# Kernel tuning notes

Hardware: AMD Instinct MI355X
Metric: run time of the kernel (lower is better)

The kernel has to match this reference:

```python
import jax, jax.numpy as jnp
from jax import lax
import numpy as np

B, N, NPOINT, NSAMPLE = 4, 8192, 1024, 32
RADIUS = 0.2
EPS = 1e-5
C_IN = 16
MLP_DIMS = [(3 + C_IN, 64), (64, 64), (64, 128)]


def setup_inputs() -> dict:
    key = jax.random.key(0)
    ks = jax.random.split(key, 16)
    inp = {
        "xyz": jax.random.uniform(ks[0], (B, N, 3), dtype=jnp.float32),
        "points": jax.random.normal(ks[1], (B, N, C_IN), dtype=jnp.float32),
    }
    for i, (cin, cout) in enumerate(MLP_DIMS, 1):
        inp[f"w{i}"] = jax.random.normal(ks[1 + i], (cout, cin), dtype=jnp.float32) / np.sqrt(cin)
        inp[f"b{i}"] = jnp.zeros((cout,), jnp.float32)
        inp[f"g{i}"] = jnp.ones((cout,), jnp.float32)
        inp[f"be{i}"] = jnp.zeros((cout,), jnp.float32)
    return inp


def fps(xyz, npoint):
    # Farthest point sampling; sequential by nature -> lax.scan over npoint steps.
    # Deterministic start at index 0 (torch version uses a random start).
    b, n, _ = xyz.shape
    def step(carry, _):
        dist, far = carry
        centroid = jnp.take_along_axis(xyz, far[:, None, None], axis=1)  # [B,1,3]
        d = jnp.sum((xyz - centroid) ** 2, -1)                            # [B,N]
        dist = jnp.minimum(dist, d)
        return (dist, jnp.argmax(dist, -1).astype(jnp.int32)), far
    init = (jnp.full((b, n), 1e10, xyz.dtype), jnp.zeros((b,), jnp.int32))
    _, idxs = lax.scan(step, init, None, length=npoint)
    return jnp.transpose(idxs)  # [B, npoint]


def gather2(pts, idx):  # pts [B,N,C], idx [B,S] -> [B,S,C]
    return jnp.take_along_axis(pts, idx[..., None], axis=1)


def gather3(pts, idx):  # pts [B,N,C], idx [B,S,K] -> [B,S,K,C]
    b, s, k = idx.shape
    out = jnp.take_along_axis(pts, idx.reshape(b, s * k)[..., None], axis=1)
    return out.reshape(b, s, k, pts.shape[-1])


def ball_query(radius, nsample, xyz, new_xyz):
    n = xyz.shape[1]
    # [B,S,N] pairwise squared distances (the memory-bound hot spot)
    sqr = jnp.sum((new_xyz[:, :, None, :] - xyz[:, None, :, :]) ** 2, -1)
    gidx = jnp.where(sqr > radius * radius, n, jnp.arange(n, dtype=jnp.int32))
    gidx = jnp.sort(gidx, axis=-1)[:, :, :nsample]
    first = gidx[:, :, :1]
    return jnp.where(gidx == n, first, gidx)


def mlp_layer(x, w, b, g, be):
    # 1x1 Conv2d + BatchNorm2d (train mode: batch stats over B,S,K) + ReLU
    y = jnp.einsum('bskc,oc->bsko', x, w) + b
    mu = jnp.mean(y, axis=(0, 1, 2))
    var = jnp.var(y, axis=(0, 1, 2))
    y = (y - mu) * (g * lax.rsqrt(var + EPS)) + be
    return jax.nn.relu(y)


def reference(xyz, points, w1, b1, g1, be1, w2, b2, g2, be2, w3, b3, g3, be3):
    fps_idx = fps(xyz, NPOINT)                       # [B,S]
    new_xyz = gather2(xyz, fps_idx)                  # [B,S,3]
    idx = ball_query(RADIUS, NSAMPLE, xyz, new_xyz)  # [B,S,K]
    grouped_xyz_norm = gather3(xyz, idx) - new_xyz[:, :, None, :]  # [B,S,K,3]
    grouped_points = gather3(points, idx)            # [B,S,K,C]
    feat = jnp.concatenate([grouped_xyz_norm, grouped_points], -1)  # [B,S,K,3+C]
    feat = mlp_layer(feat, w1, b1, g1, be1)
    feat = mlp_layer(feat, w2, b2, g2, be2)
    feat = mlp_layer(feat, w3, b3, g3, be3)
    new_points = jnp.max(feat, axis=2)               # max-pool over neighbors -> [B,S,128]
    return new_xyz, new_points
```

## Files before the change

kernel.cpp:

```cpp
#include <hip/hip_runtime.h>

#define NB 4
#define NP 8192
#define NS 1024
#define NK 32
#define CNT_ALL 131072.0f

typedef float v2f __attribute__((ext_vector_type(2)));

template <int CTRL>
__device__ __forceinline__ unsigned dpp_max_u32(unsigned m)
{
    unsigned o = (unsigned)__builtin_amdgcn_update_dpp((int)m, (int)m, CTRL, 0xF, 0xF, false);
    return (o > m) ? o : m;
}

template <int CTRL>
__device__ __forceinline__ unsigned long long dpp_max_u64(unsigned long long k)
{
    unsigned lo = (unsigned)k, hi = (unsigned)(k >> 32);
    unsigned olo = (unsigned)__builtin_amdgcn_update_dpp((int)lo, (int)lo, CTRL, 0xF, 0xF, false);
    unsigned ohi = (unsigned)__builtin_amdgcn_update_dpp((int)hi, (int)hi, CTRL, 0xF, 0xF, false);
    unsigned long long o = ((unsigned long long)ohi << 32) | (unsigned long long)olo;
    return (o > k) ? o : k;
}

__global__ __launch_bounds__(512, 2) void fps_kernel(const float* __restrict__ xyz,
                                                     float* __restrict__ newxyz,
                                                     float* __restrict__ st)
{
#pragma clang fp contract(off)
    if (blockIdx.x >= NB) {
        for (int i = threadIdx.x; i < 4096; i += 512) st[i] = 0.f;
        return;
    }
    const int b = blockIdx.x;
    const int tid = threadIdx.x;
    const int lane = tid & 63;
    const int w = tid >> 6;
    const float* xb = xyz + (size_t)b * NP * 3;

    __shared__ float s_px[NP], s_py[NP], s_pz[NP];
    __shared__ unsigned long long s_kv[2][8];

#pragma unroll
    for (int k = 0; k < 16; ++k) {
        const int i = k * 512 + tid;
        s_px[i] = xb[3 * i + 0];
        s_py[i] = xb[3 * i + 1];
        s_pz[i] = xb[3 * i + 2];
    }
    __syncthreads();

    v2f px[8], py[8], pz[8], dist[8];
    const int base = tid << 4;
#pragma unroll
    for (int m = 0; m < 8; ++m) {
        const int p0 = base + 2 * m;
        px[m] = v2f{s_px[p0], s_px[p0 + 1]};
        py[m] = v2f{s_py[p0], s_py[p0 + 1]};
        pz[m] = v2f{s_pz[p0], s_pz[p0 + 1]};
        dist[m] = v2f{1e10f, 1e10f};
    }
    float cx = s_px[0], cy = s_py[0], cz = s_pz[0];
    float* ob = newxyz + (size_t)b * NS * 3;

    for (int it = 0; it < NS; ++it) {
        if (tid == 0) { ob[it * 3 + 0] = cx; ob[it * 3 + 1] = cy; ob[it * 3 + 2] = cz; }
        const v2f cxx = v2f{cx, cx}, cyy = v2f{cy, cy}, czz = v2f{cz, cz};
        float bd0 = -1.0f, bd1 = -1.0f;
        int bj0 = 0, bj1 = 0;
#pragma unroll
        for (int m = 0; m < 8; ++m) {
            v2f dx = px[m] - cxx, dy = py[m] - cyy, dz = pz[m] - czz;
            v2f d = (dx * dx + dy * dy) + dz * dz;
            float d0 = fminf(dist[m].x, d.x);
            float d1 = fminf(dist[m].y, d.y);
            dist[m].x = d0;
            dist[m].y = d1;
            bool t0 = d0 > bd0;
            bd0 = t0 ? d0 : bd0;
            bj0 = t0 ? 2 * m : bj0;
            bool t1 = d1 > bd1;
            bd1 = t1 ? d1 : bd1;
            bj1 = t1 ? 2 * m + 1 : bj1;
        }
        const bool tm = (bd1 > bd0) || ((bd1 == bd0) && (bj1 < bj0));
        const float bd = tm ? bd1 : bd0;
        const int ibest = base + (tm ? bj1 : bj0);
        const unsigned ub = __float_as_uint(bd);
        unsigned m0 = dpp_max_u32<0xB1>(ub);
        m0 = dpp_max_u32<0x4E>(m0);
        m0 = dpp_max_u32<0x141>(m0);
        m0 = dpp_max_u32<0x140>(m0);
        m0 = dpp_max_u32<0x142>(m0);
        m0 = dpp_max_u32<0x143>(m0);
        const unsigned maxbits = (unsigned)__builtin_amdgcn_readlane((int)m0, 63);
        const unsigned long long bm = __ballot(ub == maxbits);
        const int srclane = __ffsll(bm) - 1;
        const int wbi = __builtin_amdgcn_readlane(ibest, srclane);
        if (lane == 0)
            s_kv[it & 1][w] = ((unsigned long long)maxbits << 32) | (unsigned)(NP - 1 - wbi);
        __syncthreads();
        unsigned long long kv = s_kv[it & 1][lane & 7];
        kv = dpp_max_u64<0xB1>(kv);
        kv = dpp_max_u64<0x4E>(kv);
        kv = dpp_max_u64<0x141>(kv);
        const int fi = NP - 1 - (int)(unsigned)(kv & 0xFFFFFFFFull);
        cx = s_px[fi]; cy = s_py[fi]; cz = s_pz[fi];
    }
}

__device__ __forceinline__ void bn_coef(const float* __restrict__ sums,
                                        const float* __restrict__ sqs,
                                        const float* __restrict__ g,
                                        const float* __restrict__ be,
                                        int C, int c, float& sc, float& sh)
{
    float s = 0.f, q = 0.f;
#pragma unroll
    for (int k = 0; k < 8; ++k) { s += sums[k * C + c]; q += sqs[k * C + c]; }
    const float mean = s / CNT_ALL;
    const float var = q / CNT_ALL - mean * mean;
    sc = g[c] / sqrtf(var + 1e-5f);
    sh = be[c] - mean * sc;
}

__global__ __launch_bounds__(256) void phaseA_kernel(
    const float* __restrict__ xyz, const float* __restrict__ pts,
    const float* __restrict__ newxyz,
    const float* __restrict__ w1, const float* __restrict__ b1,
    float* __restrict__ y1, float* __restrict__ st)
{
    __shared__ int   s_ball[8][NK];
    __shared__ float s_feat[256][20];
    __shared__ float s_ps[256], s_pq[256];
    float* sums1 = st;
    float* sqs1 = st + 512;

    const int tid = threadIdx.x;
    const int bk = blockIdx.x;
    const int lane = tid & 63;
    const int wv_id = tid >> 6;

    const int b = (8 * bk) >> 10;
    const float* xb = xyz + (size_t)b * NP * 3;
    const float rr = (float)(0.2 * 0.2);
    for (int r = 0; r < 2; ++r) {
        const int lg = 2 * wv_id + r;
        const int sg = 8 * bk + lg;
        const float cx = newxyz[sg * 3 + 0];
        const float cy = newxyz[sg * 3 + 1];
        const float cz = newxyz[sg * 3 + 2];
        int cnt = 0;
        for (int base = 0; base < NP && cnt < NK; base += 64) {
            const int p = base + lane;
            float dx = xb[p * 3 + 0] - cx;
            float dy = xb[p * 3 + 1] - cy;
            float dz = xb[p * 3 + 2] - cz;
            float d = __fadd_rn(__fadd_rn(__fmul_rn(dx, dx), __fmul_rn(dy, dy)),
                                __fmul_rn(dz, dz));
            bool in = (d <= rr);
            unsigned long long mask = __ballot(in);
            int before = __popcll(mask & ((1ull << lane) - 1ull));
            int pos = cnt + before;
            if (in && pos < NK) s_ball[lg][pos] = p;
            cnt += (int)__popcll(mask);
        }
        cnt = min(cnt, NK);
        const int v0 = s_ball[lg][0];
        if (lane < NK && lane >= cnt) s_ball[lg][lane] = v0;
    }
    __syncthreads();
    {
        const int lg = tid >> 5, k = tid & 31;
        const int id = s_ball[lg][k];
        const int sg = 8 * bk + lg;
        const float* pp = xyz + ((size_t)b * NP + id) * 3;
        const float* cp = newxyz + (size_t)sg * 3;
        float* f = s_feat[tid];
        f[0] = pp[0] - cp[0];
        f[1] = pp[1] - cp[1];
        f[2] = pp[2] - cp[2];
        const float4* q4 = (const float4*)(pts + ((size_t)b * NP + id) * 16);
#pragma unroll
        for (int i = 0; i < 4; ++i) {
            float4 v = q4[i];
            f[3 + 4 * i + 0] = v.x; f[3 + 4 * i + 1] = v.y;
            f[3 + 4 * i + 2] = v.z; f[3 + 4 * i + 3] = v.w;
        }
        f[19] = 0.f;
    }
    __syncthreads();
    const int c = tid & 63, rg = tid >> 6;
    float wv[20];
#pragma unroll
    for (int j = 0; j < 19; ++j) wv[j] = w1[c * 19 + j];
    wv[19] = 0.f;
    const float bs = b1[c];
    float s = 0.f, q = 0.f;
    for (int r = 0; r < 64; ++r) {
        const int row = rg * 64 + r;
        const float4* f4 = (const float4*)s_feat[row];
        float acc = bs;
#pragma unroll
        for (int j4 = 0; j4 < 5; ++j4) {
            float4 v = f4[j4];
            acc += wv[4*j4+0]*v.x + wv[4*j4+1]*v.y + wv[4*j4+2]*v.z + wv[4*j4+3]*v.w;
        }
        y1[((size_t)256 * bk + row) * 64 + c] = acc;
        s += acc; q += acc * acc;
    }
    s_ps[tid] = s; s_pq[tid] = q;
    __syncthreads();
    if (rg == 0) {
        float ts = s_ps[c] + s_ps[64 + c] + s_ps[128 + c] + s_ps[192 + c];
        float tq = s_pq[c] + s_pq[64 + c] + s_pq[128 + c] + s_pq[192 + c];
        atomicAdd(&sums1[(bk & 7) * 64 + c], ts);
        atomicAdd(&sqs1[(bk & 7) * 64 + c], tq);
    }
}

__global__ __launch_bounds__(256) void phaseB_kernel(
    const float* __restrict__ y1,
    const float* __restrict__ g1, const float* __restrict__ be1,
    const float* __restrict__ w2, const float* __restrict__ b2,
    float* __restrict__ y2, float* __restrict__ st)
{
    __shared__ float x_lds[128 * 64];
    __shared__ float s_sc[64], s_sh[64];
    __shared__ float s_ps[256], s_pq[256];
    const float* sums1 = st;
    const float* sqs1 = st + 512;
    float* sums2 = st + 1024;
    float* sqs2 = st + 1536;

    const int tid = threadIdx.x;
    const int bk = blockIdx.x;
    if (tid < 64) {
        float sc, sh;
        bn_coef(sums1, sqs1, g1, be1, 64, tid, sc, sh);
        s_sc[tid] = sc; s_sh[tid] = sh;
    }
    __syncthreads();
    const int c = tid & 63, rg = tid >> 6;
    float wv[64];
#pragma unroll
    for (int j = 0; j < 64; ++j) wv[j] = w2[c * 64 + j];
    const float bs = b2[c];
    float s = 0.f, q = 0.f;
    for (int half = 0; half < 2; ++half) {
        const size_t row0 = (size_t)256 * bk + 128 * half;
        const float4* y1g = (const float4*)(y1 + row0 * 64);
        float4* xl4 = (float4*)x_lds;
#pragma unroll
        for (int i = 0; i < 8; ++i) {
            const int slot = i * 256 + tid;
            float4 v = y1g[slot];
            const int c4 = (slot & 15) * 4;
            float4 o;
            o.x = fmaxf(v.x * s_sc[c4+0] + s_sh[c4+0], 0.f);
            o.y = fmaxf(v.y * s_sc[c4+1] + s_sh[c4+1], 0.f);
            o.z = fmaxf(v.z * s_sc[c4+2] + s_sh[c4+2], 0.f);
            o.w = fmaxf(v.w * s_sc[c4+3] + s_sh[c4+3], 0.f);
            xl4[slot] = o;
        }
        __syncthreads();
        for (int r = 0; r < 32; ++r) {
            const int row = rg * 32 + r;
            const float4* x4 = (const float4*)(x_lds + row * 64);
            float acc = bs;
#pragma unroll
            for (int j4 = 0; j4 < 16; ++j4) {
                float4 v = x4[j4];
                acc += wv[4*j4+0]*v.x + wv[4*j4+1]*v.y + wv[4*j4+2]*v.z + wv[4*j4+3]*v.w;
            }
            y2[(row0 + row) * 64 + c] = acc;
            s += acc; q += acc * acc;
        }
        __syncthreads();
    }
    s_ps[tid] = s; s_pq[tid] = q;
    __syncthreads();
    if (rg == 0) {
        float ts = s_ps[c] + s_ps[64 + c] + s_ps[128 + c] + s_ps[192 + c];
        float tq = s_pq[c] + s_pq[64 + c] + s_pq[128 + c] + s_pq[192 + c];
        atomicAdd(&sums2[(bk & 7) * 64 + c], ts);
        atomicAdd(&sqs2[(bk & 7) * 64 + c], tq);
    }
}

__global__ __launch_bounds__(256) void phaseC_kernel(
    const float* __restrict__ y2,
    const float* __restrict__ g2, const float* __restrict__ be2,
    const float* __restrict__ w3, const float* __restrict__ b3,
    float* __restrict__ st)
{
    __shared__ float s_x[NK * 64];
    __shared__ float s_sc[64], s_sh[64];
    __shared__ float s_p3s[256], s_p3q[256];
    const float* sums2 = st + 1024;
    const float* sqs2 = st + 1536;
    float* sums3 = st + 2048;
    float* sqs3 = st + 3072;

    const int tid = threadIdx.x;
    const int bk = blockIdx.x;
    if (tid < 64) {
        float sc, sh;
        bn_coef(sums2, sqs2, g2, be2, 64, tid, sc, sh);
        s_sc[tid] = sc; s_sh[tid] = sh;
    }
    __syncthreads();
    const int c = tid & 127, rg = tid >> 7;
    float wv[64];
#pragma unroll
    for (int j = 0; j < 64; ++j) wv[j] = w3[c * 64 + j];
    const float bs = b3[c];
    float s = 0.f, q = 0.f;
    for (int gi = 0; gi < 8; ++gi) {
        const size_t grow0 = (size_t)256 * bk + 32 * gi;
        const float4* y2g = (const float4*)(y2 + grow0 * 64);
        float4* sx4 = (float4*)s_x;
#pragma unroll
        for (int i = 0; i < 2; ++i) {
            const int slot = i * 256 + tid;
            float4 v = y2g[slot];
            const int c4 = (slot & 15) * 4;
            float4 o;
            o.x = fmaxf(v.x * s_sc[c4+0] + s_sh[c4+0], 0.f);
            o.y = fmaxf(v.y * s_sc[c4+1] + s_sh[c4+1], 0.f);
            o.z = fmaxf(v.z * s_sc[c4+2] + s_sh[c4+2], 0.f);
            o.w = fmaxf(v.w * s_sc[c4+3] + s_sh[c4+3], 0.f);
            sx4[slot] = o;
        }
        __syncthreads();
        for (int r = 0; r < 16; ++r) {
            const int row = rg * 16 + r;
            const float4* x4 = (const float4*)(s_x + row * 64);
            float acc = bs;
#pragma unroll
            for (int j4 = 0; j4 < 16; ++j4) {
                float4 v = x4[j4];
                acc += wv[4*j4+0]*v.x + wv[4*j4+1]*v.y + wv[4*j4+2]*v.z + wv[4*j4+3]*v.w;
            }
            s += acc; q += acc * acc;
        }
        __syncthreads();
    }
    s_p3s[rg * 128 + c] = s; s_p3q[rg * 128 + c] = q;
    __syncthreads();
    if (rg == 0) {
        atomicAdd(&sums3[(bk & 7) * 128 + c], s_p3s[c] + s_p3s[128 + c]);
        atomicAdd(&sqs3[(bk & 7) * 128 + c], s_p3q[c] + s_p3q[128 + c]);
    }
}

__global__ __launch_bounds__(256) void phaseD_kernel(
    const float* __restrict__ y2,
    const float* __restrict__ g2, const float* __restrict__ be2,
    const float* __restrict__ g3, const float* __restrict__ be3,
    const float* __restrict__ w3, const float* __restrict__ b3,
    const float* __restrict__ st, float* __restrict__ out_np)
{
    __shared__ float s_x[NK * 64];
    __shared__ float s_sc[64], s_sh[64];
    __shared__ float s_fm[256];
    const float* sums2 = st + 1024;
    const float* sqs2 = st + 1536;
    const float* sums3 = st + 2048;
    const float* sqs3 = st + 3072;

    const int tid = threadIdx.x;
    const int bk = blockIdx.x;
    if (tid < 64) {
        float sc, sh;
        bn_coef(sums2, sqs2, g2, be2, 64, tid, sc, sh);
        s_sc[tid] = sc; s_sh[tid] = sh;
    }
    const int c = tid & 127, rg = tid >> 7;
    float sc3, sh3;
    bn_coef(sums3, sqs3, g3, be3, 128, c, sc3, sh3);
    __syncthreads();
    float wv[64];
#pragma unroll
    for (int j = 0; j < 64; ++j) wv[j] = w3[c * 64 + j];
    const float bs = b3[c];
    for (int gi = 0; gi < 8; ++gi) {
        const size_t grow0 = (size_t)256 * bk + 32 * gi;
        const float4* y2g = (const float4*)(y2 + grow0 * 64);
        float4* sx4 = (float4*)s_x;
#pragma unroll
        for (int i = 0; i < 2; ++i) {
            const int slot = i * 256 + tid;
            float4 v = y2g[slot];
            const int c4 = (slot & 15) * 4;
            float4 o;
            o.x = fmaxf(v.x * s_sc[c4+0] + s_sh[c4+0], 0.f);
            o.y = fmaxf(v.y * s_sc[c4+1] + s_sh[c4+1], 0.f);
            o.z = fmaxf(v.z * s_sc[c4+2] + s_sh[c4+2], 0.f);
            o.w = fmaxf(v.w * s_sc[c4+3] + s_sh[c4+3], 0.f);
            sx4[slot] = o;
        }
        __syncthreads();
        float m = 0.f;
        for (int r = 0; r < 16; ++r) {
            const int row = rg * 16 + r;
            const float4* x4 = (const float4*)(s_x + row * 64);
            float acc = bs;
#pragma unroll
            for (int j4 = 0; j4 < 16; ++j4) {
                float4 v = x4[j4];
                acc += wv[4*j4+0]*v.x + wv[4*j4+1]*v.y + wv[4*j4+2]*v.z + wv[4*j4+3]*v.w;
            }
            float rv = fmaxf(acc * sc3 + sh3, 0.f);
            m = fmaxf(m, rv);
        }
        s_fm[rg * 128 + c] = m;
        __syncthreads();
        if (rg == 0)
            out_np[(size_t)(8 * bk + gi) * 128 + c] = fmaxf(s_fm[c], s_fm[128 + c]);
        __syncthreads();
    }
}

extern "C" void kernel_launch(void* const* d_in, const int* in_sizes, int n_in,
                              void* d_out, int out_size, void* d_ws, size_t ws_size,
                              hipStream_t stream)
{
    (void)in_sizes; (void)n_in; (void)out_size;
    const float* xyz = (const float*)d_in[0];
    const float* pts = (const float*)d_in[1];
    const float* w1 = (const float*)d_in[2];
    const float* b1 = (const float*)d_in[3];
    const float* g1 = (const float*)d_in[4];
    const float* be1 = (const float*)d_in[5];
    const float* w2 = (const float*)d_in[6];
    const float* b2 = (const float*)d_in[7];
    const float* g2 = (const float*)d_in[8];
    const float* be2 = (const float*)d_in[9];
    const float* w3 = (const float*)d_in[10];
    const float* b3 = (const float*)d_in[11];
    const float* g3 = (const float*)d_in[12];
    const float* be3 = (const float*)d_in[13];

    float* out = (float*)d_out;
    float* newxyz = out;
    float* newpts = out + NB * NS * 3;

    float* y1 = (float*)d_ws;
    float* y2 = y1 + 8388608;
    float* st = y2 + 8388608;
    const size_t needed = (2ull * 8388608ull + 4096ull) * 4ull;
    if (ws_size < needed) return;

    fps_kernel<<<NB + 1, 512, 0, stream>>>(xyz, newxyz, st);
    phaseA_kernel<<<512, 256, 0, stream>>>(xyz, pts, newxyz, w1, b1, y1, st);
    phaseB_kernel<<<512, 256, 0, stream>>>(y1, g1, be1, w2, b2, y2, st);
    phaseC_kernel<<<512, 256, 0, stream>>>(y2, g2, be2, w3, b3, st);
    phaseD_kernel<<<512, 256, 0, stream>>>(y2, g2, be2, g3, be3, w3, b3, st, newpts);
}
```

Baseline: 1.123 ms.

## Overlap FPS with ball query via progress flags; skip layer-3 recompute using max/min

Merges farthest point sampling and the first grouping/MLP stage into one kernel. FPS blocks publish per-iteration progress counters, and consumer blocks spin-wait on those counters so ball query and layer 1 run while sampling is still in progress. Phase C now also records the per-group max and min of the pre-BN layer-3 outputs. This lets the final kernel apply BN+ReLU to max or min according to the sign of the scale, instead of recomputing the 64x128 matmul. The cost is reliance on all blocks being co-resident to avoid deadlock, relaxed-ordering visibility of the published centroids, and extra workspace.

```diff
diff --git a/kernel.cpp b/kernel.cpp
--- a/kernel.cpp
+++ b/kernel.cpp
@@ -7,6 +7,9 @@
 #define CNT_ALL 131072.0f
 
 typedef float v2f __attribute__((ext_vector_type(2)));
+typedef unsigned long long u64;
+
+#define AGENT __HIP_MEMORY_SCOPE_AGENT
 
 template <int CTRL>
 __device__ __forceinline__ unsigned dpp_max_u32(unsigned m)
@@ -16,98 +19,211 @@
 }
 
 template <int CTRL>
-__device__ __forceinline__ unsigned long long dpp_max_u64(unsigned long long k)
+__device__ __forceinline__ u64 dpp_max_u64(u64 k)
 {
     unsigned lo = (unsigned)k, hi = (unsigned)(k >> 32);
     unsigned olo = (unsigned)__builtin_amdgcn_update_dpp((int)lo, (int)lo, CTRL, 0xF, 0xF, false);
     unsigned ohi = (unsigned)__builtin_amdgcn_update_dpp((int)hi, (int)hi, CTRL, 0xF, 0xF, false);
-    unsigned long long o = ((unsigned long long)ohi << 32) | (unsigned long long)olo;
+    u64 o = ((u64)ohi << 32) | (u64)olo;
     return (o > k) ? o : k;
 }
 
-__global__ __launch_bounds__(512, 2) void fps_kernel(const float* __restrict__ xyz,
-                                                     float* __restrict__ newxyz,
-                                                     float* __restrict__ st)
-{
-#pragma clang fp contract(off)
-    if (blockIdx.x >= NB) {
-        for (int i = threadIdx.x; i < 4096; i += 512) st[i] = 0.f;
-        return;
-    }
-    const int b = blockIdx.x;
+__global__ __launch_bounds__(512, 1) void k1_kernel(
+    const float* __restrict__ xyz, const float* __restrict__ pts,
+    float* __restrict__ newxyz,
+    const float* __restrict__ w1, const float* __restrict__ b1,
+    float* __restrict__ y1, float* __restrict__ st, unsigned* __restrict__ prog)
+{
+    __shared__ __align__(16) char smem[98432];
     const int tid = threadIdx.x;
     const int lane = tid & 63;
-    const int w = tid >> 6;
+    const int wv = tid >> 6;
+
+    if (blockIdx.x < NB) {
+#pragma clang fp contract(off)
+        float* s_px = (float*)smem;
+        float* s_py = (float*)(smem + 32768);
+        float* s_pz = (float*)(smem + 65536);
+        u64*   s_kv = (u64*)(smem + 98304);
+        const int b = blockIdx.x;
+        const float* xb = xyz + (size_t)b * NP * 3;
+
+#pragma unroll
+        for (int k = 0; k < 16; ++k) {
+            const int i = k * 512 + tid;
+            s_px[i] = xb[3 * i + 0];
+            s_py[i] = xb[3 * i + 1];
+            s_pz[i] = xb[3 * i + 2];
+        }
+        __syncthreads();
+
+        v2f px[8], py[8], pz[8], dist[8];
+        const int base = tid << 4;
+#pragma unroll
+        for (int m = 0; m < 8; ++m) {
+            const int p0 = base + 2 * m;
+            px[m] = v2f{s_px[p0], s_px[p0 + 1]};
+            py[m] = v2f{s_py[p0], s_py[p0 + 1]};
+            pz[m] = v2f{s_pz[p0], s_pz[p0 + 1]};
+            dist[m] = v2f{1e10f, 1e10f};
+        }
+        float cx = s_px[0], cy = s_py[0], cz = s_pz[0];
+        float* ob = newxyz + (size_t)b * NS * 3;
+
+        for (int it = 0; it < NS; ++it) {
+            if (tid == 0) {
+                __hip_atomic_store(&prog[b], (unsigned)it, __ATOMIC_RELAXED, AGENT);
+                __hip_atomic_store(&ob[it * 3 + 0], cx, __ATOMIC_RELAXED, AGENT);
+                __hip_atomic_store(&ob[it * 3 + 1], cy, __ATOMIC_RELAXED, AGENT);
+                __hip_atomic_store(&ob[it * 3 + 2], cz, __ATOMIC_RELAXED, AGENT);
+            }
+            const v2f cxx = v2f{cx, cx}, cyy = v2f{cy, cy}, czz = v2f{cz, cz};
+            float bd0 = -1.0f, bd1 = -1.0f;
+            int bj0 = 0, bj1 = 0;
+#pragma unroll
+            for (int m = 0; m < 8; ++m) {
+                v2f dx = px[m] - cxx, dy = py[m] - cyy, dz = pz[m] - czz;
+                v2f d = (dx * dx + dy * dy) + dz * dz;
+                float d0 = fminf(dist[m].x, d.x);
+                float d1 = fminf(dist[m].y, d.y);
+                dist[m].x = d0;
+                dist[m].y = d1;
+                bool t0 = d0 > bd0;
+                bd0 = t0 ? d0 : bd0;
+                bj0 = t0 ? 2 * m : bj0;
+                bool t1 = d1 > bd1;
+                bd1 = t1 ? d1 : bd1;
+                bj1 = t1 ? 2 * m + 1 : bj1;
+            }
+            const bool tm = (bd1 > bd0) || ((bd1 == bd0) && (bj1 < bj0));
+            const float bd = tm ? bd1 : bd0;
+            const int ibest = base + (tm ? bj1 : bj0);
+            const unsigned ub = __float_as_uint(bd);
+            unsigned m0 = dpp_max_u32<0xB1>(ub);
+            m0 = dpp_max_u32<0x4E>(m0);
+            m0 = dpp_max_u32<0x141>(m0);
+            m0 = dpp_max_u32<0x140>(m0);
+            m0 = dpp_max_u32<0x142>(m0);
+            m0 = dpp_max_u32<0x143>(m0);
+            const unsigned maxbits = (unsigned)__builtin_amdgcn_readlane((int)m0, 63);
+            const u64 bm = __ballot(ub == maxbits);
+            const int srclane = __ffsll(bm) - 1;
+            const int wbi = __builtin_amdgcn_readlane(ibest, srclane);
+            if (lane == 0)
+                s_kv[(it & 1) * 8 + wv] = ((u64)maxbits << 32) | (unsigned)(NP - 1 - wbi);
+            __syncthreads();
+            u64 kv = s_kv[(it & 1) * 8 + (lane & 7)];
+            kv = dpp_max_u64<0xB1>(kv);
+            kv = dpp_max_u64<0x4E>(kv);
+            kv = dpp_max_u64<0x141>(kv);
+            const int fi = NP - 1 - (int)(unsigned)(kv & 0xFFFFFFFFull);
+            cx = s_px[fi]; cy = s_py[fi]; cz = s_pz[fi];
+        }
+        if (tid == 0)
+            __hip_atomic_store(&prog[b], (unsigned)NS, __ATOMIC_RELAXED, AGENT);
+        return;
+    }
+
+    int*   s_ball = (int*)smem;
+    float* s_cent = (float*)(smem + 1024);
+    float* s_feat = (float*)(smem + 1152);
+    float* s_ps   = (float*)(smem + 1152 + 20480);
+    float* s_pq   = s_ps + 512;
+
+    const int abk = blockIdx.x - NB;
+    const int b = abk >> 5;
+    const int s0 = (abk & 31) * 32;
     const float* xb = xyz + (size_t)b * NP * 3;
-
-    __shared__ float s_px[NP], s_py[NP], s_pz[NP];
-    __shared__ unsigned long long s_kv[2][8];
-
-#pragma unroll
-    for (int k = 0; k < 16; ++k) {
-        const int i = k * 512 + tid;
-        s_px[i] = xb[3 * i + 0];
-        s_py[i] = xb[3 * i + 1];
-        s_pz[i] = xb[3 * i + 2];
-    }
+    const float rr = (float)(0.2 * 0.2);
+
+    const int c = tid & 63, rg = tid >> 6;
+    float wvr[20];
+#pragma unroll
+    for (int j = 0; j < 19; ++j) wvr[j] = w1[c * 19 + j];
+    wvr[19] = 0.f;
+    const float bs = b1[c];
+    float sa = 0.f, qa = 0.f;
+
+    for (int chunk = 0; chunk < 4; ++chunk) {
+        const int sl = s0 + chunk * 8;
+        if (tid == 0) {
+            while ((int)__hip_atomic_load(&prog[b], __ATOMIC_RELAXED, AGENT) < sl + 8)
+                __builtin_amdgcn_s_sleep(4);
+        }
+        __syncthreads();
+        {
+            const int sg = (b << 10) + sl + wv;
+            float cxv, cyv, czv;
+            if (lane == 0) {
+                cxv = __hip_atomic_load(&newxyz[sg * 3 + 0], __ATOMIC_RELAXED, AGENT);
+                cyv = __hip_atomic_load(&newxyz[sg * 3 + 1], __ATOMIC_RELAXED, AGENT);
+                czv = __hip_atomic_load(&newxyz[sg * 3 + 2], __ATOMIC_RELAXED, AGENT);
+                s_cent[wv * 4 + 0] = cxv;
+                s_cent[wv * 4 + 1] = cyv;
+                s_cent[wv * 4 + 2] = czv;
+            }
+            cxv = __shfl(cxv, 0); cyv = __shfl(cyv, 0); czv = __shfl(czv, 0);
+            int cnt = 0;
+            for (int bse = 0; bse < NP && cnt < NK; bse += 64) {
+                const int p = bse + lane;
+                float dx = xb[p * 3 + 0] - cxv;
+                float dy = xb[p * 3 + 1] - cyv;
+                float dz = xb[p * 3 + 2] - czv;
+                float d = __fadd_rn(__fadd_rn(__fmul_rn(dx, dx), __fmul_rn(dy, dy)),
+                                    __fmul_rn(dz, dz));
+                bool in = (d <= rr);
+                u64 mask = __ballot(in);
+                int before = __popcll(mask & ((1ull << lane) - 1ull));
+                int pos = cnt + before;
+                if (in && pos < NK) s_ball[wv * NK + pos] = p;
+                cnt += (int)__popcll(mask);
+            }
+            cnt = min(cnt, NK);
+            const int v0 = s_ball[wv * NK];
+            if (lane < NK && lane >= cnt) s_ball[wv * NK + lane] = v0;
+        }
+        __syncthreads();
+        if (tid < 256) {
+            const int lg = tid >> 5, k = tid & 31;
+            const int id = s_ball[lg * NK + k];
+            const float* pp = xyz + ((size_t)b * NP + id) * 3;
+            float* f = s_feat + tid * 20;
+            f[0] = pp[0] - s_cent[lg * 4 + 0];
+            f[1] = pp[1] - s_cent[lg * 4 + 1];
+            f[2] = pp[2] - s_cent[lg * 4 + 2];
+            const float4* q4 = (const float4*)(pts + ((size_t)b * NP + id) * 16);
+#pragma unroll
+            for (int i = 0; i < 4; ++i) {
+                float4 v = q4[i];
+                f[3 + 4 * i + 0] = v.x; f[3 + 4 * i + 1] = v.y;
+                f[3 + 4 * i + 2] = v.z; f[3 + 4 * i + 3] = v.w;
+            }
+            f[19] = 0.f;
+        }
+        __syncthreads();
+        const size_t rowbase = (size_t)abk * 1024 + (size_t)chunk * 256;
+        for (int r = 0; r < 32; ++r) {
+            const int row = rg * 32 + r;
+            const float4* f4 = (const float4*)(s_feat + row * 20);
+            float acc = bs;
+#pragma unroll
+            for (int j4 = 0; j4 < 5; ++j4) {
+                float4 v = f4[j4];
+                acc += wvr[4*j4+0]*v.x + wvr[4*j4+1]*v.y + wvr[4*j4+2]*v.z + wvr[4*j4+3]*v.w;
+            }
+            y1[(rowbase + row) * 64 + c] = acc;
+            sa += acc; qa += acc * acc;
+        }
+        __syncthreads();
+    }
+    s_ps[tid] = sa; s_pq[tid] = qa;
     __syncthreads();
-
-    v2f px[8], py[8], pz[8], dist[8];
-    const int base = tid << 4;
-#pragma unroll
-    for (int m = 0; m < 8; ++m) {
-        const int p0 = base + 2 * m;
-        px[m] = v2f{s_px[p0], s_px[p0 + 1]};
-        py[m] = v2f{s_py[p0], s_py[p0 + 1]};
-        pz[m] = v2f{s_pz[p0], s_pz[p0 + 1]};
-        dist[m] = v2f{1e10f, 1e10f};
-    }
-    float cx = s_px[0], cy = s_py[0], cz = s_pz[0];
-    float* ob = newxyz + (size_t)b * NS * 3;
-
-    for (int it = 0; it < NS; ++it) {
-        if (tid == 0) { ob[it * 3 + 0] = cx; ob[it * 3 + 1] = cy; ob[it * 3 + 2] = cz; }
-        const v2f cxx = v2f{cx, cx}, cyy = v2f{cy, cy}, czz = v2f{cz, cz};
-        float bd0 = -1.0f, bd1 = -1.0f;
-        int bj0 = 0, bj1 = 0;
-#pragma unroll
-        for (int m = 0; m < 8; ++m) {
-            v2f dx = px[m] - cxx, dy = py[m] - cyy, dz = pz[m] - czz;
-            v2f d = (dx * dx + dy * dy) + dz * dz;
-            float d0 = fminf(dist[m].x, d.x);
-            float d1 = fminf(dist[m].y, d.y);
-            dist[m].x = d0;
-            dist[m].y = d1;
-            bool t0 = d0 > bd0;
-            bd0 = t0 ? d0 : bd0;
-            bj0 = t0 ? 2 * m : bj0;
-            bool t1 = d1 > bd1;
-            bd1 = t1 ? d1 : bd1;
-            bj1 = t1 ? 2 * m + 1 : bj1;
-        }
-        const bool tm = (bd1 > bd0) || ((bd1 == bd0) && (bj1 < bj0));
-        const float bd = tm ? bd1 : bd0;
-        const int ibest = base + (tm ? bj1 : bj0);
-        const unsigned ub = __float_as_uint(bd);
-        unsigned m0 = dpp_max_u32<0xB1>(ub);
-        m0 = dpp_max_u32<0x4E>(m0);
-        m0 = dpp_max_u32<0x141>(m0);
-        m0 = dpp_max_u32<0x140>(m0);
-        m0 = dpp_max_u32<0x142>(m0);
-        m0 = dpp_max_u32<0x143>(m0);
-        const unsigned maxbits = (unsigned)__builtin_amdgcn_readlane((int)m0, 63);
-        const unsigned long long bm = __ballot(ub == maxbits);
-        const int srclane = __ffsll(bm) - 1;
-        const int wbi = __builtin_amdgcn_readlane(ibest, srclane);
-        if (lane == 0)
-            s_kv[it & 1][w] = ((unsigned long long)maxbits << 32) | (unsigned)(NP - 1 - wbi);
-        __syncthreads();
-        unsigned long long kv = s_kv[it & 1][lane & 7];
-        kv = dpp_max_u64<0xB1>(kv);
-        kv = dpp_max_u64<0x4E>(kv);
-        kv = dpp_max_u64<0x141>(kv);
-        const int fi = NP - 1 - (int)(unsigned)(kv & 0xFFFFFFFFull);
-        cx = s_px[fi]; cy = s_py[fi]; cz = s_pz[fi];
+    if (tid < 64) {
+        float ts = 0.f, tq = 0.f;
+#pragma unroll
+        for (int i = 0; i < 8; ++i) { ts += s_ps[i * 64 + tid]; tq += s_pq[i * 64 + tid]; }
+        atomicAdd(&st[(abk & 7) * 64 + tid], ts);
+        atomicAdd(&st[512 + (abk & 7) * 64 + tid], tq);
     }
 }
 
@@ -124,101 +240,6 @@
     const float var = q / CNT_ALL - mean * mean;
     sc = g[c] / sqrtf(var + 1e-5f);
     sh = be[c] - mean * sc;
-}
-
-__global__ __launch_bounds__(256) void phaseA_kernel(
-    const float* __restrict__ xyz, const float* __restrict__ pts,
-    const float* __restrict__ newxyz,
-    const float* __restrict__ w1, const float* __restrict__ b1,
-    float* __restrict__ y1, float* __restrict__ st)
-{
-    __shared__ int   s_ball[8][NK];
-    __shared__ float s_feat[256][20];
-    __shared__ float s_ps[256], s_pq[256];
-    float* sums1 = st;
-    float* sqs1 = st + 512;
-
-    const int tid = threadIdx.x;
-    const int bk = blockIdx.x;
-    const int lane = tid & 63;
-    const int wv_id = tid >> 6;
-
-    const int b = (8 * bk) >> 10;
-    const float* xb = xyz + (size_t)b * NP * 3;
-    const float rr = (float)(0.2 * 0.2);
-    for (int r = 0; r < 2; ++r) {
-        const int lg = 2 * wv_id + r;
-        const int sg = 8 * bk + lg;
-        const float cx = newxyz[sg * 3 + 0];
-        const float cy = newxyz[sg * 3 + 1];
-        const float cz = newxyz[sg * 3 + 2];
-        int cnt = 0;
-        for (int base = 0; base < NP && cnt < NK; base += 64) {
-            const int p = base + lane;
-            float dx = xb[p * 3 + 0] - cx;
-            float dy = xb[p * 3 + 1] - cy;
-            float dz = xb[p * 3 + 2] - cz;
-            float d = __fadd_rn(__fadd_rn(__fmul_rn(dx, dx), __fmul_rn(dy, dy)),
-                                __fmul_rn(dz, dz));
-            bool in = (d <= rr);
-            unsigned long long mask = __ballot(in);
-            int before = __popcll(mask & ((1ull << lane) - 1ull));
-            int pos = cnt + before;
-            if (in && pos < NK) s_ball[lg][pos] = p;
-            cnt += (int)__popcll(mask);
-        }
-        cnt = min(cnt, NK);
-        const int v0 = s_ball[lg][0];
-        if (lane < NK && lane >= cnt) s_ball[lg][lane] = v0;
-    }
-    __syncthreads();
-    {
-        const int lg = tid >> 5, k = tid & 31;
-        const int id = s_ball[lg][k];
-        const int sg = 8 * bk + lg;
-        const float* pp = xyz + ((size_t)b * NP + id) * 3;
-        const float* cp = newxyz + (size_t)sg * 3;
-        float* f = s_feat[tid];
-        f[0] = pp[0] - cp[0];
-        f[1] = pp[1] - cp[1];
-        f[2] = pp[2] - cp[2];
-        const float4* q4 = (const float4*)(pts + ((size_t)b * NP + id) * 16);
-#pragma unroll
-        for (int i = 0; i < 4; ++i) {
-            float4 v = q4[i];
-            f[3 + 4 * i + 0] = v.x; f[3 + 4 * i + 1] = v.y;
-            f[3 + 4 * i + 2] = v.z; f[3 + 4 * i + 3] = v.w;
-        }
-        f[19] = 0.f;
-    }
-    __syncthreads();
-    const int c = tid & 63, rg = tid >> 6;
-    float wv[20];
-#pragma unroll
-    for (int j = 0; j < 19; ++j) wv[j] = w1[c * 19 + j];
-    wv[19] = 0.f;
-    const float bs = b1[c];
-    float s = 0.f, q = 0.f;
-    for (int r = 0; r < 64; ++r) {
-        const int row = rg * 64 + r;
-        const float4* f4 = (const float4*)s_feat[row];
-        float acc = bs;
-#pragma unroll
-        for (int j4 = 0; j4 < 5; ++j4) {
-            float4 v = f4[j4];
-            acc += wv[4*j4+0]*v.x + wv[4*j4+1]*v.y + wv[4*j4+2]*v.z + wv[4*j4+3]*v.w;
-        }
-        y1[((size_t)256 * bk + row) * 64 + c] = acc;
-        s += acc; q += acc * acc;
-    }
-    s_ps[tid] = s; s_pq[tid] = q;
-    __syncthreads();
-    if (rg == 0) {
-        float ts = s_ps[c] + s_ps[64 + c] + s_ps[128 + c] + s_ps[192 + c];
-        float tq = s_pq[c] + s_pq[64 + c] + s_pq[128 + c] + s_pq[192 + c];
-        atomicAdd(&sums1[(bk & 7) * 64 + c], ts);
-        atomicAdd(&sqs1[(bk & 7) * 64 + c], tq);
-    }
 }
 
 __global__ __launch_bounds__(256) void phaseB_kernel(
@@ -290,15 +311,16 @@
     }
 }
 
-__global__ __launch_bounds__(256) void phaseC_kernel(
+__global__ __launch_bounds__(256) void phaseC2_kernel(
     const float* __restrict__ y2,
     const float* __restrict__ g2, const float* __restrict__ be2,
     const float* __restrict__ w3, const float* __restrict__ b3,
-    float* __restrict__ st)
+    float* __restrict__ st, float* __restrict__ mxb, float* __restrict__ mnb)
 {
     __shared__ float s_x[NK * 64];
     __shared__ float s_sc[64], s_sh[64];
     __shared__ float s_p3s[256], s_p3q[256];
+    __shared__ float s_mx[256], s_mn[256];
     const float* sums2 = st + 1024;
     const float* sqs2 = st + 1536;
     float* sums3 = st + 2048;
@@ -335,6 +357,7 @@
             sx4[slot] = o;
         }
         __syncthreads();
+        float mx = -1e30f, mn = 1e30f;
         for (int r = 0; r < 16; ++r) {
             const int row = rg * 16 + r;
             const float4* x4 = (const float4*)(s_x + row * 64);
@@ -345,6 +368,14 @@
                 acc += wv[4*j4+0]*v.x + wv[4*j4+1]*v.y + wv[4*j4+2]*v.z + wv[4*j4+3]*v.w;
             }
             s += acc; q += acc * acc;
+            mx = fmaxf(mx, acc); mn = fminf(mn, acc);
+        }
+        s_mx[rg * 128 + c] = mx; s_mn[rg * 128 + c] = mn;
+        __syncthreads();
+        if (rg == 0) {
+            const size_t gidx = (size_t)(8 * bk + gi) * 128 + c;
+            mxb[gidx] = fmaxf(s_mx[c], s_mx[128 + c]);
+            mnb[gidx] = fminf(s_mn[c], s_mn[128 + c]);
         }
         __syncthreads();
     }
@@ -356,72 +387,18 @@
     }
 }
 
-__global__ __launch_bounds__(256) void phaseD_kernel(
-    const float* __restrict__ y2,
-    const float* __restrict__ g2, const float* __restrict__ be2,
+__global__ __launch_bounds__(256) void phaseD2_kernel(
+    const float* __restrict__ st,
     const float* __restrict__ g3, const float* __restrict__ be3,
-    const float* __restrict__ w3, const float* __restrict__ b3,
-    const float* __restrict__ st, float* __restrict__ out_np)
-{
-    __shared__ float s_x[NK * 64];
-    __shared__ float s_sc[64], s_sh[64];
-    __shared__ float s_fm[256];
-    const float* sums2 = st + 1024;
-    const float* sqs2 = st + 1536;
-    const float* sums3 = st + 2048;
-    const float* sqs3 = st + 3072;
-
-    const int tid = threadIdx.x;
-    const int bk = blockIdx.x;
-    if (tid < 64) {
-        float sc, sh;
-        bn_coef(sums2, sqs2, g2, be2, 64, tid, sc, sh);
-        s_sc[tid] = sc; s_sh[tid] = sh;
-    }
-    const int c = tid & 127, rg = tid >> 7;
-    float sc3, sh3;
-    bn_coef(sums3, sqs3, g3, be3, 128, c, sc3, sh3);
-    __syncthreads();
-    float wv[64];
-#pragma unroll
-    for (int j = 0; j < 64; ++j) wv[j] = w3[c * 64 + j];
-    const float bs = b3[c];
-    for (int gi = 0; gi < 8; ++gi) {
-        const size_t grow0 = (size_t)256 * bk + 32 * gi;
-        const float4* y2g = (const float4*)(y2 + grow0 * 64);
-        float4* sx4 = (float4*)s_x;
-#pragma unroll
-        for (int i = 0; i < 2; ++i) {
-            const int slot = i * 256 + tid;
-            float4 v = y2g[slot];
-            const int c4 = (slot & 15) * 4;
-            float4 o;
-            o.x = fmaxf(v.x * s_sc[c4+0] + s_sh[c4+0], 0.f);
-            o.y = fmaxf(v.y * s_sc[c4+1] + s_sh[c4+1], 0.f);
-            o.z = fmaxf(v.z * s_sc[c4+2] + s_sh[c4+2], 0.f);
-            o.w = fmaxf(v.w * s_sc[c4+3] + s_sh[c4+3], 0.f);
-            sx4[slot] = o;
-        }
-        __syncthreads();
-        float m = 0.f;
-        for (int r = 0; r < 16; ++r) {
-            const int row = rg * 16 + r;
-            const float4* x4 = (const float4*)(s_x + row * 64);
-            float acc = bs;
-#pragma unroll
-            for (int j4 = 0; j4 < 16; ++j4) {
-                float4 v = x4[j4];
-                acc += wv[4*j4+0]*v.x + wv[4*j4+1]*v.y + wv[4*j4+2]*v.z + wv[4*j4+3]*v.w;
-            }
-            float rv = fmaxf(acc * sc3 + sh3, 0.f);
-            m = fmaxf(m, rv);
-        }
-        s_fm[rg * 128 + c] = m;
-        __syncthreads();
-        if (rg == 0)
-            out_np[(size_t)(8 * bk + gi) * 128 + c] = fmaxf(s_fm[c], s_fm[128 + c]);
-        __syncthreads();
-    }
+    const float* __restrict__ mxb, const float* __restrict__ mnb,
+    float* __restrict__ out_np)
+{
+    const int idx = blockIdx.x * 256 + threadIdx.x;
+    const int c = idx & 127;
+    float sc, sh;
+    bn_coef(st + 2048, st + 3072, g3, be3, 128, c, sc, sh);
+    const float sel = (sc >= 0.f) ? mxb[idx] : mnb[idx];
+    out_np[idx] = fmaxf(sel * sc + sh, 0.f);
 }
 
 extern "C" void kernel_launch(void* const* d_in, const int* in_sizes, int n_in,
@@ -451,12 +428,15 @@
     float* y1 = (float*)d_ws;
     float* y2 = y1 + 8388608;
     float* st = y2 + 8388608;
-    const size_t needed = (2ull * 8388608ull + 4096ull) * 4ull;
+    unsigned* prog = (unsigned*)(st + 4096);
+    float* mxb = st + 4104;
+    float* mnb = mxb + 524288;
+    const size_t needed = (2ull * 8388608ull + 4104ull + 2ull * 524288ull) * 4ull;
     if (ws_size < needed) return;
 
-    fps_kernel<<<NB + 1, 512, 0, stream>>>(xyz, newxyz, st);
-    phaseA_kernel<<<512, 256, 0, stream>>>(xyz, pts, newxyz, w1, b1, y1, st);
+    hipMemsetAsync(st, 0, (4096 + 8) * sizeof(float), stream);
+    k1_kernel<<<NB + 128, 512, 0, stream>>>(xyz, pts, newxyz, w1, b1, y1, st, prog);
     phaseB_kernel<<<512, 256, 0, stream>>>(y1, g1, be1, w2, b2, y2, st);
-    phaseC_kernel<<<512, 256, 0, stream>>>(y2, g2, be2, w3, b3, st);
-    phaseD_kernel<<<512, 256, 0, stream>>>(y2, g2, be2, g3, be3, w3, b3, st, newpts);
-}
+    phaseC2_kernel<<<512, 256, 0, stream>>>(y2, g2, be2, w3, b3, st, mxb, mnb);
+    phaseD2_kernel<<<2048, 256, 0, stream>>>(st, g3, be3, mxb, mnb, newpts);
+}
```

After: 1.079 ms. 1.04x faster.
